# Optimization experiments

Hardware: AMD Instinct MI355X
Metric: run time of the kernel (lower is better)

Reference implementation:

```python
import jax, jax.numpy as jnp
import numpy as np

NUM_HARMONICS = 64
SAMPLE_RATE = 48000
TWO_PI = 2.0 * np.pi


def setup_inputs() -> dict:
    key = jax.random.key(0)
    k1, k2, k3 = jax.random.split(key, 3)
    B, N, H = 8, 96000, NUM_HARMONICS
    # f0 in a realistic vocal/instrument range ~ [80, 480] Hz
    f0_hz = 80.0 + 400.0 * jax.random.uniform(k1, (B, N), dtype=jnp.float32)
    amp_harm = jax.random.uniform(k2, (B, N, H), dtype=jnp.float32)
    phase = jax.random.normal(k3, (B, H), dtype=jnp.float32)
    return {"f0_hz": f0_hz, "amp_harm": amp_harm, "phase": phase}


def reference(f0_hz, amp_harm, phase):
    # f0_hz: (B, N); amp_harm: (B, N, H); phase: (B, H)
    H = amp_harm.shape[-1]
    omega = (TWO_PI / SAMPLE_RATE) * f0_hz                      # (B, N)
    harm_idx = jnp.arange(1, H + 1, dtype=f0_hz.dtype)          # (H,)
    omega_h = omega[..., None] * harm_idx                       # (B, N, H)
    phases = jnp.cumsum(omega_h, axis=1) + phase[:, None, :]    # (B, N, H)
    y = jnp.einsum('bnh,bnh->bn', amp_harm, jnp.sin(phases))    # (B, N)
    phase_out = jnp.remainder(phases[:, -1, :], TWO_PI)         # (B, H)
    return (y, phase_out)
```

## Files before the change

### kernel.cpp

```cpp
#include <hip/hip_runtime.h>
#include <cstdint>
#include <cstddef>


#define B   8
#define N   96000
#define H   64
#define CH  768
#define NCH 125
#define G   3
#define PF  8

static_assert(CH * NCH == N, "chunking");
static_assert(G * 256 == CH, "scan layout");
static_assert(NCH <= 128, "predecessor sum uses 2 loads/lane");

static constexpr double TWO_PI_D     = 6.2831853071795864769252867665590057684;
static constexpr double INV_TWO_PI_D = 1.0 / TWO_PI_D;
static constexpr double OMEGA_D      = TWO_PI_D / 48000.0;

__device__ __forceinline__ float wrap2pi_f(double v) {
  double r = v - TWO_PI_D * floor(v * INV_TWO_PI_D);
  return (float)r;
}

__global__ __launch_bounds__(256) void k_chunk_sums(const float* __restrict__ f0,
                                                    double* __restrict__ csum) {
  const int blk = blockIdx.x;
  const int b = blk / NCH, c = blk - b * NCH;
  const float* p = f0 + (size_t)b * N + (size_t)c * CH;
  const int tid = threadIdx.x;

  double s = 0.0;
#pragma unroll
  for (int j = 0; j < G; ++j) s += OMEGA_D * (double)p[tid + j * 256];

  for (int off = 32; off > 0; off >>= 1) s += __shfl_down(s, off);

  __shared__ double sw[4];
  const int lane = tid & 63, wv = tid >> 6;
  if (lane == 0) sw[wv] = s;
  __syncthreads();
  if (tid == 0) csum[blk] = sw[0] + sw[1] + sw[2] + sw[3];
}

__global__ __launch_bounds__(256) void k_main(const float* __restrict__ f0,
                                              const float* __restrict__ amp,
                                              const float* __restrict__ phase,
                                              const double* __restrict__ csum,
                                              float* __restrict__ out) {
  const int blk = blockIdx.x;
  const int b = blk / NCH, c = blk - b * NCH;
  const int tid = threadIdx.x;
  const int lane = tid & 63, wv = tid >> 6;
  const size_t base = (size_t)b * N + (size_t)c * CH;

  __shared__ float  s_w[CH];
  __shared__ double s_warp[4];
  __shared__ double s_pre;
  __shared__ double s_last;

  const float* f0p = f0 + base;
  const float f0v0 = f0p[tid * G + 0];
  const float f0v1 = f0p[tid * G + 1];
  const float f0v2 = f0p[tid * G + 2];

  const int hq = lane & 15;
  const int sl = lane >> 4;
  const float4* ampb = reinterpret_cast<const float4*>(amp) + base * (H / 4);
  float4 pf[PF];
#pragma unroll
  for (int j = 0; j < PF; ++j) {
    const int nl = j * 16 + (wv << 2) + sl;
    pf[j] = ampb[(size_t)nl * (H / 4) + hq];
  }

  if (wv == 0) {
    double pre = 0.0;
    if (lane < c)      pre  = csum[b * NCH + lane];
    if (lane + 64 < c) pre += csum[b * NCH + lane + 64];
    for (int off = 32; off > 0; off >>= 1) pre += __shfl_xor(pre, off);
    if (lane == 0) s_pre = pre;
  }

  const double l0 = OMEGA_D * (double)f0v0;
  const double l1 = OMEGA_D * (double)f0v1;
  const double l2 = OMEGA_D * (double)f0v2;
  const double ts = l0 + l1 + l2;

  double x = ts;
#pragma unroll
  for (int off = 1; off < 64; off <<= 1) {
    double y = __shfl_up(x, off);
    if (lane >= off) x += y;
  }
  if (lane == 63) s_warp[wv] = x;
  __syncthreads();
  if (tid == 0) {
    double a = 0.0;
#pragma unroll
    for (int w = 0; w < 4; ++w) { double t = s_warp[w]; s_warp[w] = a; a += t; }
  }
  __syncthreads();

  const double run = s_pre + s_warp[wv] + (x - ts);
  const double o0 = run + l0;
  const double o1 = o0 + l1;
  const double o2 = o1 + l2;
  s_w[tid * G + 0] = wrap2pi_f(o0);
  s_w[tid * G + 1] = wrap2pi_f(o1);
  s_w[tid * G + 2] = wrap2pi_f(o2);
  if (tid == 255) s_last = o2;
  __syncthreads();

  const float m0 = (float)(hq * 4 + 1), m1 = (float)(hq * 4 + 2);
  const float m2 = (float)(hq * 4 + 3), m3 = (float)(hq * 4 + 4);
  const float* phb = phase + b * H;
  const float p0 = phb[hq * 4 + 0], p1 = phb[hq * 4 + 1];
  const float p2 = phb[hq * 4 + 2], p3 = phb[hq * 4 + 3];
  float* yb = out + base;

#pragma unroll
  for (int j = 0; j < PF; ++j) {
    const int nl = j * 16 + (wv << 2) + sl;
    const float w = s_w[nl];
    const float4 a4 = pf[j];
    float acc;
    acc  = a4.x * __sinf(fmaf(w, m0, p0));
    acc += a4.y * __sinf(fmaf(w, m1, p1));
    acc += a4.z * __sinf(fmaf(w, m2, p2));
    acc += a4.w * __sinf(fmaf(w, m3, p3));
    acc += __shfl_xor(acc, 1);
    acc += __shfl_xor(acc, 2);
    acc += __shfl_xor(acc, 4);
    acc += __shfl_xor(acc, 8);
    if (hq == 0) yb[nl] = acc;
  }

#pragma unroll 4
  for (int i0 = PF * 16; i0 < CH; i0 += 16) {
    const int nl = i0 + (wv << 2) + sl;
    const float w = s_w[nl];
    const float4 a4 = ampb[(size_t)nl * (H / 4) + hq];
    float acc;
    acc  = a4.x * __sinf(fmaf(w, m0, p0));
    acc += a4.y * __sinf(fmaf(w, m1, p1));
    acc += a4.z * __sinf(fmaf(w, m2, p2));
    acc += a4.w * __sinf(fmaf(w, m3, p3));
    acc += __shfl_xor(acc, 1);
    acc += __shfl_xor(acc, 2);
    acc += __shfl_xor(acc, 4);
    acc += __shfl_xor(acc, 8);
    if (hq == 0) yb[nl] = acc;
  }

  if (c == NCH - 1 && tid < H) {
    const double arg = s_last * (double)(tid + 1) + (double)phase[b * H + tid];
    double r = arg - TWO_PI_D * floor(arg * INV_TWO_PI_D);
    if (r < 0.0) r += TWO_PI_D;
    if (r >= TWO_PI_D) r -= TWO_PI_D;
    out[(size_t)B * N + b * H + tid] = (float)r;
  }
}

extern "C" void kernel_launch(void* const* d_in, const int* in_sizes, int n_in,
                              void* d_out, int out_size, void* d_ws, size_t ws_size,
                              hipStream_t stream) {
  const float* f0    = (const float*)d_in[0];
  const float* amp   = (const float*)d_in[1];
  const float* phase = (const float*)d_in[2];
  float* out = (float*)d_out;
  double* csum = (double*)d_ws;

  k_chunk_sums<<<B * NCH, 256, 0, stream>>>(f0, csum);
  k_main<<<B * NCH, 256, 0, stream>>>(f0, amp, phase, csum, out);
}
```

Before: 40.32 us.

## Fuse chunk-sum and main kernels with decoupled lookback spin on chunk sums

Merges the chunk-sum pre-pass into the main kernel. Each block publishes its chunk total with a release atomic store, then spins with acquire loads until all predecessor totals are nonzero. A memset zeroes the workspace before launch. This removes a second kernel launch and a full extra read of f0, but it depends on predecessor blocks being resident, since forward progress is not guaranteed. It also treats an exact zero sum as not ready, and it halves the amp prefetch depth.

Measured after the change: 76.08 us. +88.7%, slower.

```diff
diff --git a/kernel.cpp b/kernel.cpp
--- a/kernel.cpp
+++ b/kernel.cpp
@@ -9,11 +9,11 @@
 #define CH  768
 #define NCH 125
 #define G   3
-#define PF  8
+#define PF  4
 
 static_assert(CH * NCH == N, "chunking");
 static_assert(G * 256 == CH, "scan layout");
-static_assert(NCH <= 128, "predecessor sum uses 2 loads/lane");
+static_assert(NCH <= 128, "predecessor spin uses 2 loads/lane");
 
 static constexpr double TWO_PI_D     = 6.2831853071795864769252867665590057684;
 static constexpr double INV_TWO_PI_D = 1.0 / TWO_PI_D;
@@ -24,31 +24,11 @@
   return (float)r;
 }
 
-__global__ __launch_bounds__(256) void k_chunk_sums(const float* __restrict__ f0,
-                                                    double* __restrict__ csum) {
-  const int blk = blockIdx.x;
-  const int b = blk / NCH, c = blk - b * NCH;
-  const float* p = f0 + (size_t)b * N + (size_t)c * CH;
-  const int tid = threadIdx.x;
-
-  double s = 0.0;
-#pragma unroll
-  for (int j = 0; j < G; ++j) s += OMEGA_D * (double)p[tid + j * 256];
-
-  for (int off = 32; off > 0; off >>= 1) s += __shfl_down(s, off);
-
-  __shared__ double sw[4];
-  const int lane = tid & 63, wv = tid >> 6;
-  if (lane == 0) sw[wv] = s;
-  __syncthreads();
-  if (tid == 0) csum[blk] = sw[0] + sw[1] + sw[2] + sw[3];
-}
-
-__global__ __launch_bounds__(256) void k_main(const float* __restrict__ f0,
-                                              const float* __restrict__ amp,
-                                              const float* __restrict__ phase,
-                                              const double* __restrict__ csum,
-                                              float* __restrict__ out) {
+__global__ __launch_bounds__(256, 4) void k_fused(const float* __restrict__ f0,
+                                                  const float* __restrict__ amp,
+                                                  const float* __restrict__ phase,
+                                                  double* __restrict__ csum,
+                                                  float* __restrict__ out) {
   const int blk = blockIdx.x;
   const int b = blk / NCH, c = blk - b * NCH;
   const int tid = threadIdx.x;
@@ -75,14 +55,6 @@
     pf[j] = ampb[(size_t)nl * (H / 4) + hq];
   }
 
-  if (wv == 0) {
-    double pre = 0.0;
-    if (lane < c)      pre  = csum[b * NCH + lane];
-    if (lane + 64 < c) pre += csum[b * NCH + lane + 64];
-    for (int off = 32; off > 0; off >>= 1) pre += __shfl_xor(pre, off);
-    if (lane == 0) s_pre = pre;
-  }
-
   const double l0 = OMEGA_D * (double)f0v0;
   const double l1 = OMEGA_D * (double)f0v1;
   const double l2 = OMEGA_D * (double)f0v2;
@@ -100,6 +72,29 @@
     double a = 0.0;
 #pragma unroll
     for (int w = 0; w < 4; ++w) { double t = s_warp[w]; s_warp[w] = a; a += t; }
+    __hip_atomic_store(&csum[blk], a, __ATOMIC_RELEASE, __HIP_MEMORY_SCOPE_AGENT);
+  }
+  __syncthreads();
+
+  if (wv == 0) {
+    const double* cs = csum + b * NCH;
+    const bool need0 = (lane < c);
+    const bool need1 = (lane + 64 < c);
+    double v0 = 0.0, v1 = 0.0;
+    for (;;) {
+      if (need0 && v0 == 0.0)
+        v0 = __hip_atomic_load(&cs[lane], __ATOMIC_ACQUIRE,
+                               __HIP_MEMORY_SCOPE_AGENT);
+      if (need1 && v1 == 0.0)
+        v1 = __hip_atomic_load(&cs[lane + 64], __ATOMIC_ACQUIRE,
+                               __HIP_MEMORY_SCOPE_AGENT);
+      const int done = ((!need0) | (v0 != 0.0)) & ((!need1) | (v1 != 0.0));
+      if (__all(done)) break;
+      __builtin_amdgcn_s_sleep(2);
+    }
+    double pre = v0 + v1;
+    for (int off = 32; off > 0; off >>= 1) pre += __shfl_xor(pre, off);
+    if (lane == 0) s_pre = pre;
   }
   __syncthreads();
 
@@ -172,6 +167,6 @@
   float* out = (float*)d_out;
   double* csum = (double*)d_ws;
 
-  k_chunk_sums<<<B * NCH, 256, 0, stream>>>(f0, csum);
-  k_main<<<B * NCH, 256, 0, stream>>>(f0, amp, phase, csum, out);
+  hipMemsetAsync(d_ws, 0, (size_t)B * NCH * sizeof(double), stream);
+  k_fused<<<B * NCH, 256, 0, stream>>>(f0, amp, phase, csum, out);
 }
```
